# Kernel optimization log

Hardware: AMD Instinct MI355X
Metric: run time of the kernel (lower is better)

## Reference

```python
import jax, jax.numpy as jnp
import numpy as np

B, S, D, FF, E = 4, 2048, 1024, 4096, 8


def setup_inputs() -> dict:
    key = jax.random.key(0)
    ks = jax.random.split(key, 6)
    scale_r = 1.0 / np.sqrt(D)
    return {
        "x": jax.random.normal(ks[0], (B, S, D), dtype=jnp.float32),
        "W_router": jax.random.normal(ks[1], (D, E), dtype=jnp.float32) * scale_r,
        "W1": jax.random.normal(ks[2], (E, D, FF), dtype=jnp.float32) * (1.0 / np.sqrt(D)),
        "b1": jnp.zeros((E, FF), dtype=jnp.float32),
        "W2": jax.random.normal(ks[3], (E, FF, D), dtype=jnp.float32) * (1.0 / np.sqrt(FF)),
        "b2": jnp.zeros((E, D), dtype=jnp.float32),
    }


def reference(x, W_router, W1, b1, W2, b2):
    # Router: softmax over experts, top-2, renormalize the 2 gates with softmax
    logits = jnp.einsum("bsd,de->bse", x, W_router)          # [B,S,E]
    probs = jax.nn.softmax(logits, axis=-1)
    top_vals, top_idx = jax.lax.top_k(probs, 2)               # [B,S,2]
    gates2 = jax.nn.softmax(top_vals, axis=-1)                # [B,S,2]

    num_experts = W1.shape[0]
    out = jnp.zeros_like(x)
    # Faithful masked-dense MoE: each expert runs over all tokens (input masked),
    # output scaled by its gate (0 for non-selected tokens).
    for i in range(num_experts):
        sel = (top_idx == i)                                  # [B,S,2] bool
        mask = jnp.any(sel, axis=-1, keepdims=True).astype(x.dtype)  # [B,S,1]
        xi = x * mask
        h = jax.nn.gelu(jnp.einsum("bsd,df->bsf", xi, W1[i]) + b1[i], approximate=False)
        yi = jnp.einsum("bsf,fd->bsd", h, W2[i]) + b2[i]
        g = jnp.sum(gates2 * sel.astype(x.dtype), axis=-1, keepdims=True)  # [B,S,1]
        out = out + yi * g
    return out
```

## Files before the change

### kernel.cpp

```cpp
#include <hip/hip_runtime.h>
#include <hip/hip_bf16.h>
#include <math.h>

#define NEXP 8
#define DDIM 1024
#define FFDIM 4096
#define NTOK 8192
#define NSLOT (NTOK * 2)
#define BM 128
#define BN 128
#define BK 64
#define MAXT ((NSLOT / BM) + NEXP)

typedef __attribute__((ext_vector_type(8))) __bf16 bf16x8;
typedef __attribute__((ext_vector_type(4))) __bf16 bf16x4;
typedef __attribute__((ext_vector_type(4))) float f32x4;

union BF8 { __bf16 b[8]; uint4 u; bf16x8 v; };

typedef const __attribute__((address_space(1))) void* gptr1_t;
typedef __attribute__((address_space(3))) void* lptr3_t;
__device__ __forceinline__ void gll16(const void* g, void* l) {
    __builtin_amdgcn_global_load_lds((gptr1_t)g, (lptr3_t)l, 16, 0, 0);
}

__device__ __forceinline__ float gelu_fast(float v) {
    float vv = v * v;
    float ex = __expf(v * fmaf(0.0713548162726f, vv, 1.59576912161f));
    float s = __builtin_amdgcn_rcpf(ex + 1.0f);
    return v * (1.0f - s);
}

__device__ __forceinline__ int swz(int row, int colb) {
    return row * 128 + (colb ^ ((row & 7) << 4));
}

__device__ __forceinline__ int xcd_logical(int bid, int nwg) {
    if (nwg & 7) return bid;
    return (bid & 7) * (nwg >> 3) + (bid >> 3);
}

__global__ __launch_bounds__(256)
void router_kernel(const float* __restrict__ x, const float* __restrict__ Wr,
                   __bf16* __restrict__ xb, int write_xb,
                   int* __restrict__ idx2, float* __restrict__ gates2,
                   int* __restrict__ counts)
{
    int tid = threadIdx.x;
    int t = blockIdx.x * 4 + (tid >> 6);
    int lane = tid & 63;
    const float* xr = x + (size_t)t * DDIM;

    float acc[NEXP];
#pragma unroll
    for (int e = 0; e < NEXP; ++e) acc[e] = 0.f;

#pragma unroll
    for (int i = 0; i < 2; ++i) {
        int d0 = i * 512 + lane * 8;
        float4 a = *(const float4*)(xr + d0);
        float4 b = *(const float4*)(xr + d0 + 4);
        float vals[8] = {a.x, a.y, a.z, a.w, b.x, b.y, b.z, b.w};
#pragma unroll
        for (int q = 0; q < 8; ++q) {
            const float* wrow = Wr + (size_t)(d0 + q) * NEXP;
#pragma unroll
            for (int e = 0; e < NEXP; ++e) acc[e] += vals[q] * wrow[e];
        }
        if (write_xb) {
            BF8 pk;
#pragma unroll
            for (int q = 0; q < 8; ++q) pk.b[q] = (__bf16)vals[q];
            *(uint4*)(xb + (size_t)t * DDIM + d0) = pk.u;
        }
    }
#pragma unroll
    for (int e = 0; e < NEXP; ++e) {
        float v = acc[e];
        for (int off = 32; off > 0; off >>= 1) v += __shfl_xor(v, off, 64);
        acc[e] = v;
    }
    if (lane == 0) {
        float mx = acc[0];
#pragma unroll
        for (int e = 1; e < NEXP; ++e) mx = fmaxf(mx, acc[e]);
        float p[NEXP]; float s = 0.f;
#pragma unroll
        for (int e = 0; e < NEXP; ++e) { p[e] = expf(acc[e] - mx); s += p[e]; }
        float inv = 1.f / s;
#pragma unroll
        for (int e = 0; e < NEXP; ++e) p[e] *= inv;
        int i1 = 0; float p1 = p[0];
#pragma unroll
        for (int e = 1; e < NEXP; ++e) if (p[e] > p1) { p1 = p[e]; i1 = e; }
        int i2 = -1; float p2 = -1.f;
#pragma unroll
        for (int e = 0; e < NEXP; ++e) {
            if (e == i1) continue;
            if (p[e] > p2) { p2 = p[e]; i2 = e; }
        }
        float u = expf(p2 - p1);
        float den = 1.f + u;
        idx2[2 * t] = i1; idx2[2 * t + 1] = i2;
        gates2[2 * t] = 1.f / den; gates2[2 * t + 1] = u / den;
        atomicAdd(&counts[i1], 1);
        atomicAdd(&counts[i2], 1);
    }
}

__global__ __launch_bounds__(256)
void offsets_kernel(const int* __restrict__ counts, int* __restrict__ offsets,
                    int* __restrict__ cursors, int* __restrict__ tiletab)
{
    __shared__ int soff[NEXP], stile[NEXP + 1];
    int tid = threadIdx.x;
    if (tid == 0) {
        int off = 0, tt = 0;
        for (int e = 0; e < NEXP; ++e) {
            soff[e] = off; stile[e] = tt;
            int c = counts[e];
            off += c; tt += (c + BM - 1) / BM;
        }
        stile[NEXP] = tt;
    }
    __syncthreads();
    if (tid < NEXP) { offsets[tid] = soff[tid]; cursors[tid] = 0; }
    int total = stile[NEXP];
    for (int i = tid; i < MAXT; i += 256) {
        if (i < total) {
            int e = 0;
            while (stile[e + 1] <= i) ++e;
            tiletab[2 * i] = e; tiletab[2 * i + 1] = i - stile[e];
        } else {
            tiletab[2 * i] = -1; tiletab[2 * i + 1] = 0;
        }
    }
}

__global__ __launch_bounds__(256)
void fill_kernel(const int* __restrict__ idx2, const float* __restrict__ gates2,
                 const int* __restrict__ offsets, int* __restrict__ cursors,
                 int* __restrict__ perm, float* __restrict__ gate_slot,
                 int* __restrict__ tslot)
{
    int t = blockIdx.x * 256 + threadIdx.x;
    if (t >= NTOK) return;
#pragma unroll
    for (int s = 0; s < 2; ++s) {
        int e = idx2[2 * t + s];
        int pos = atomicAdd(&cursors[e], 1);
        int slot = offsets[e] + pos;
        perm[slot] = t;
        gate_slot[slot] = gates2[2 * t + s];
        tslot[2 * t + s] = slot;
    }
}

__global__ __launch_bounds__(128)
void convert_w_kernel(const float* __restrict__ W, __bf16* __restrict__ WT, int K, int N)
{
    int ktiles = K >> 6;
    int nt = blockIdx.x / ktiles;
    int kt = blockIdx.x % ktiles;
    int e = blockIdx.y;
    const float* We = W + (size_t)e * K * N;
    int r = threadIdx.x;
    const float* src = We + (size_t)(kt * 64) * N + nt * 128 + r;
    char* dst = (char*)WT + ((((size_t)e * (N >> 7) + nt) * ktiles + kt) << 14) + r * 128;
    float f[64];
#pragma unroll
    for (int j = 0; j < 64; ++j) f[j] = src[(size_t)j * N];
#pragma unroll
    for (int gi = 0; gi < 8; ++gi) {
        BF8 pk;
#pragma unroll
        for (int q = 0; q < 8; ++q) pk.b[q] = (__bf16)f[gi * 8 + q];
        *(uint4*)(dst + ((gi * 16) ^ ((r & 7) << 4))) = pk.u;
    }
}

__device__ __forceinline__ bool tile_header(const int* counts, const int* offsets,
                                            const int* tiletab, int e_arg, int c_arg, int CH,
                                            int tile_idx,
                                            int& e, int& start, int& cnt, int& hbase, int& row0,
                                            int& rows_here)
{
    int rowtile;
    if (e_arg >= 0) {
        e = e_arg;
        int cbase = c_arg * CH;
        cnt = counts[e] - cbase;
        if (cnt <= 0) return false;
        if (cnt > CH) cnt = CH;
        start = offsets[e] + cbase;
        rowtile = tile_idx;
        hbase = start;
    } else {
        e = tiletab[2 * tile_idx];
        if (e < 0) return false;
        rowtile = tiletab[2 * tile_idx + 1];
        start = offsets[e];
        cnt = counts[e];
        hbase = 0;
    }
    row0 = rowtile * BM;
    if (row0 >= cnt) return false;
    rows_here = cnt - row0;
    if (rows_here > BM) rows_here = BM;
    return true;
}

__global__ __launch_bounds__(256)
void gemm1_fast(const __bf16* __restrict__ xb, const __bf16* __restrict__ W1T,
                const float* __restrict__ b1,
                const int* __restrict__ perm, const int* __restrict__ counts,
                const int* __restrict__ offsets, const int* __restrict__ tiletab,
                __bf16* __restrict__ H, int e_arg, int c_arg, int CH)
{
    __shared__ __align__(16) char smem[(BM + BN) * 128];
    char* As = smem;
    char* Bs = smem + BM * 128;

    int e, start, cnt, hbase, row0, rows_here;
    if (!tile_header(counts, offsets, tiletab, e_arg, c_arg, CH, blockIdx.y,
                     e, start, cnt, hbase, row0, rows_here))
        return;

    const float* b1e = b1 + (size_t)e * FFDIM;
    int nt = blockIdx.x;
    int n0 = nt * BN;
    const char* bsrc = (const char*)W1T + ((((size_t)e * (FFDIM >> 7) + nt) * (DDIM >> 6)) << 14);

    int tid = threadIdx.x;
    int lane = tid & 63;
    int wid = tid >> 6;
    int wm = wid >> 1, wn = wid & 1;
    int lr = lane & 15, lhi = lane >> 4;

    int ar = tid >> 1, ach = tid & 1;
    int token = -1;
    if (ar < rows_here) token = perm[start + row0 + ar];
    const __bf16* arow = xb + (size_t)(token < 0 ? 0 : token) * DDIM + ach * 32;

    const char* bwave = bsrc + wid * 4096 + lane * 16;
    char* bldsb = Bs + wid * 4096;

    f32x4 acc[4][4] = {};

    for (int kt = 0; kt < DDIM / BK; ++kt) {
        __syncthreads();
#pragma unroll
        for (int j = 0; j < 4; ++j)
            gll16(bwave + ((size_t)kt << 14) + j * 1024, bldsb + j * 1024);
        {
            uint4 v[4];
            if (token >= 0) {
                const uint4* p = (const uint4*)(arow + kt * BK);
#pragma unroll
                for (int i = 0; i < 4; ++i) v[i] = p[i];
            } else {
#pragma unroll
                for (int i = 0; i < 4; ++i) v[i] = make_uint4(0u, 0u, 0u, 0u);
            }
#pragma unroll
            for (int i = 0; i < 4; ++i)
                *(uint4*)(As + swz(ar, ach * 64 + i * 16)) = v[i];
        }
        __syncthreads();

#pragma unroll
        for (int kk = 0; kk < 2; ++kk) {
            bf16x8 af[4], bfr[4];
#pragma unroll
            for (int m = 0; m < 4; ++m)
                af[m] = *(const bf16x8*)(As + swz(wm * 64 + m * 16 + lr, kk * 64 + lhi * 16));
#pragma unroll
            for (int n = 0; n < 4; ++n)
                bfr[n] = *(const bf16x8*)(Bs + swz(wn * 64 + n * 16 + lr, kk * 64 + lhi * 16));
#pragma unroll
            for (int m = 0; m < 4; ++m)
#pragma unroll
                for (int n = 0; n < 4; ++n)
                    acc[m][n] = __builtin_amdgcn_mfma_f32_16x16x32_bf16(af[m], bfr[n], acc[m][n], 0, 0, 0);
        }
    }

    float bias[4];
#pragma unroll
    for (int n = 0; n < 4; ++n) bias[n] = b1e[n0 + wn * 64 + n * 16 + lr];

#pragma unroll
    for (int m = 0; m < 4; ++m) {
        int rbase = wm * 64 + m * 16 + lhi * 4;
#pragma unroll
        for (int j = 0; j < 4; ++j) {
            int rl = rbase + j;
            if (rl < rows_here) {
                __bf16* hr = H + (size_t)(start + row0 + rl - hbase) * FFDIM + n0 + wn * 64;
#pragma unroll
                for (int n = 0; n < 4; ++n) {
                    float v = acc[m][n][j] + bias[n];
                    hr[n * 16 + lr] = (__bf16)gelu_fast(v);
                }
            }
        }
    }
}

__global__ __launch_bounds__(256)
void gemm2_fast(const __bf16* __restrict__ H, const __bf16* __restrict__ W2T,
                const float* __restrict__ b2,
                const int* __restrict__ perm, const float* __restrict__ gate_slot,
                const int* __restrict__ counts, const int* __restrict__ offsets,
                const int* __restrict__ tiletab,
                float* __restrict__ out, __bf16* __restrict__ Y, int use_y,
                int e_arg, int c_arg, int CH)
{
    __shared__ __align__(16) char smem[(BM + BN) * 128];
    char* As = smem;
    char* Bs = smem + BM * 128;

    const int NTN = DDIM / BN;
    int tile_idx, nt;
    if (e_arg >= 0) { nt = blockIdx.x; tile_idx = blockIdx.y; }
    else {
        int L = xcd_logical(blockIdx.x, gridDim.x);
        nt = L % NTN;
        tile_idx = L / NTN;
    }

    int e, start, cnt, hbase, row0, rows_here;
    if (!tile_header(counts, offsets, tiletab, e_arg, c_arg, CH, tile_idx,
                     e, start, cnt, hbase, row0, rows_here))
        return;

    const float* b2e = b2 + (size_t)e * DDIM;
    int n0 = nt * BN;
    const char* bsrc = (const char*)W2T + ((((size_t)e * (DDIM >> 7) + nt) * (FFDIM >> 6)) << 14);

    int tid = threadIdx.x;
    int lane = tid & 63;
    int wid = tid >> 6;
    int wm = wid >> 1, wn = wid & 1;
    int lr = lane & 15, lhi = lane >> 4;

    int ar = tid >> 1, ach = tid & 1;
    bool aval = (ar < rows_here);
    const __bf16* hrow = H + (size_t)(aval ? (start + row0 + ar - hbase) : 0) * FFDIM + ach * 32;

    const char* bwave = bsrc + wid * 4096 + lane * 16;
    char* bldsb = Bs + wid * 4096;

    f32x4 acc[4][4] = {};

    for (int kt = 0; kt < FFDIM / BK; ++kt) {
        __syncthreads();
#pragma unroll
        for (int j = 0; j < 4; ++j)
            gll16(bwave + ((size_t)kt << 14) + j * 1024, bldsb + j * 1024);
        {
            uint4 v[4];
            if (aval) {
                const uint4* p = (const uint4*)(hrow + kt * BK);
#pragma unroll
                for (int i = 0; i < 4; ++i) v[i] = p[i];
            } else {
#pragma unroll
                for (int i = 0; i < 4; ++i) v[i] = make_uint4(0u, 0u, 0u, 0u);
            }
#pragma unroll
            for (int i = 0; i < 4; ++i)
                *(uint4*)(As + swz(ar, ach * 64 + i * 16)) = v[i];
        }
        __syncthreads();

#pragma unroll
        for (int kk = 0; kk < 2; ++kk) {
            bf16x8 af[4], bfr[4];
#pragma unroll
            for (int m = 0; m < 4; ++m)
                af[m] = *(const bf16x8*)(As + swz(wm * 64 + m * 16 + lr, kk * 64 + lhi * 16));
#pragma unroll
            for (int n = 0; n < 4; ++n)
                bfr[n] = *(const bf16x8*)(Bs + swz(wn * 64 + n * 16 + lr, kk * 64 + lhi * 16));
#pragma unroll
            for (int m = 0; m < 4; ++m)
#pragma unroll
                for (int n = 0; n < 4; ++n)
                    acc[m][n] = __builtin_amdgcn_mfma_f32_16x16x32_bf16(af[m], bfr[n], acc[m][n], 0, 0, 0);
        }
    }

    float bias[4];
#pragma unroll
    for (int n = 0; n < 4; ++n) bias[n] = b2e[n0 + wn * 64 + n * 16 + lr];

#pragma unroll
    for (int m = 0; m < 4; ++m) {
        int rbase = wm * 64 + m * 16 + lhi * 4;
#pragma unroll
        for (int j = 0; j < 4; ++j) {
            int rl = rbase + j;
            if (rl < rows_here) {
                int slot = start + row0 + rl;
                float g = gate_slot[slot];
                if (use_y) {
                    __bf16* yrow = Y + (size_t)slot * DDIM + n0 + wn * 64;
#pragma unroll
                    for (int n = 0; n < 4; ++n)
                        yrow[n * 16 + lr] = (__bf16)((acc[m][n][j] + bias[n]) * g);
                } else {
                    int token = perm[slot];
                    float* orow = out + (size_t)token * DDIM + n0 + wn * 64;
#pragma unroll
                    for (int n = 0; n < 4; ++n)
                        atomicAdd(orow + n * 16 + lr, (acc[m][n][j] + bias[n]) * g);
                }
            }
        }
    }
}

__global__ __launch_bounds__(256)
void combine_kernel(const __bf16* __restrict__ Y, const int* __restrict__ tslot,
                    float* __restrict__ out)
{
    int t = blockIdx.x;
    int c = threadIdx.x * 4;
    int sa = tslot[2 * t], sb = tslot[2 * t + 1];
    bf16x4 a = *(const bf16x4*)(Y + (size_t)sa * DDIM + c);
    bf16x4 b = *(const bf16x4*)(Y + (size_t)sb * DDIM + c);
    float4 r;
    r.x = (float)a[0] + (float)b[0];
    r.y = (float)a[1] + (float)b[1];
    r.z = (float)a[2] + (float)b[2];
    r.w = (float)a[3] + (float)b[3];
    *(float4*)(out + (size_t)t * DDIM + c) = r;
}

__global__ __launch_bounds__(256)
void gemm1_legacy(const float* __restrict__ x, const float* __restrict__ W1,
                  const float* __restrict__ b1,
                  const int* __restrict__ perm, const int* __restrict__ counts,
                  const int* __restrict__ offsets, const int* __restrict__ tiletab,
                  __bf16* __restrict__ H, int e_arg, int c_arg, int CH)
{
    __shared__ __align__(16) char smem[(BM + BN) * 128];
    char* As = smem;
    char* Bs = smem + BM * 128;

    int e, start, cnt, hbase, row0, rows_here;
    if (!tile_header(counts, offsets, tiletab, e_arg, c_arg, CH, blockIdx.y,
                     e, start, cnt, hbase, row0, rows_here))
        return;

    const float* W1e = W1 + (size_t)e * DDIM * FFDIM;
    const float* b1e = b1 + (size_t)e * FFDIM;
    int n0 = blockIdx.x * BN;

    int tid = threadIdx.x;
    int lane = tid & 63;
    int wid = tid >> 6;
    int wm = wid >> 1, wn = wid & 1;
    int lr = lane & 15, lhi = lane >> 4;

    int ar = tid >> 1, ach = tid & 1;
    int token = -1;
    if (ar < rows_here) token = perm[start + row0 + ar];
    const float* arow = x + (size_t)(token < 0 ? 0 : token) * DDIM + ach * 32;

    int bn = tid & 127, bkh = tid >> 7;
    const float* bcol = W1e + (size_t)bkh * 32 * FFDIM + n0 + bn;

    f32x4 acc[4][4] = {};

    for (int k0 = 0; k0 < DDIM; k0 += BK) {
        __syncthreads();
        {
            BF8 pk[4];
            if (token >= 0) {
                const float4* p = (const float4*)(arow + k0);
#pragma unroll
                for (int i = 0; i < 4; ++i) {
                    float4 v0 = p[2 * i], v1 = p[2 * i + 1];
                    pk[i].b[0] = (__bf16)v0.x; pk[i].b[1] = (__bf16)v0.y;
                    pk[i].b[2] = (__bf16)v0.z; pk[i].b[3] = (__bf16)v0.w;
                    pk[i].b[4] = (__bf16)v1.x; pk[i].b[5] = (__bf16)v1.y;
                    pk[i].b[6] = (__bf16)v1.z; pk[i].b[7] = (__bf16)v1.w;
                }
            } else {
#pragma unroll
                for (int i = 0; i < 4; ++i) pk[i].u = make_uint4(0u, 0u, 0u, 0u);
            }
#pragma unroll
            for (int i = 0; i < 4; ++i)
                *(uint4*)(As + swz(ar, ach * 64 + i * 16)) = pk[i].u;
        }
        {
            float f[32];
            const float* p = bcol + (size_t)k0 * FFDIM;
#pragma unroll
            for (int j = 0; j < 32; ++j) f[j] = p[(size_t)j * FFDIM];
#pragma unroll
            for (int i = 0; i < 4; ++i) {
                BF8 pk;
#pragma unroll
                for (int q = 0; q < 8; ++q) pk.b[q] = (__bf16)f[i * 8 + q];
                *(uint4*)(Bs + swz(bn, bkh * 64 + i * 16)) = pk.u;
            }
        }
        __syncthreads();

#pragma unroll
        for (int kk = 0; kk < 2; ++kk) {
            bf16x8 af[4], bfr[4];
#pragma unroll
            for (int m = 0; m < 4; ++m)
                af[m] = *(const bf16x8*)(As + swz(wm * 64 + m * 16 + lr, kk * 64 + lhi * 16));
#pragma unroll
            for (int n = 0; n < 4; ++n)
                bfr[n] = *(const bf16x8*)(Bs + swz(wn * 64 + n * 16 + lr, kk * 64 + lhi * 16));
#pragma unroll
            for (int m = 0; m < 4; ++m)
#pragma unroll
                for (int n = 0; n < 4; ++n)
                    acc[m][n] = __builtin_amdgcn_mfma_f32_16x16x32_bf16(af[m], bfr[n], acc[m][n], 0, 0, 0);
        }
    }

    float bias[4];
#pragma unroll
    for (int n = 0; n < 4; ++n) bias[n] = b1e[n0 + wn * 64 + n * 16 + lr];

#pragma unroll
    for (int m = 0; m < 4; ++m) {
        int rbase = wm * 64 + m * 16 + lhi * 4;
#pragma unroll
        for (int j = 0; j < 4; ++j) {
            int rl = rbase + j;
            if (rl < rows_here) {
                __bf16* hr = H + (size_t)(start + row0 + rl - hbase) * FFDIM + n0 + wn * 64;
#pragma unroll
                for (int n = 0; n < 4; ++n) {
                    float v = acc[m][n][j] + bias[n];
                    hr[n * 16 + lr] = (__bf16)gelu_fast(v);
                }
            }
        }
    }
}

__global__ __launch_bounds__(256)
void gemm2_legacy(const __bf16* __restrict__ H, const float* __restrict__ W2,
                  const float* __restrict__ b2,
                  const int* __restrict__ perm, const float* __restrict__ gate_slot,
                  const int* __restrict__ counts, const int* __restrict__ offsets,
                  const int* __restrict__ tiletab,
                  float* __restrict__ out, int e_arg, int c_arg, int CH)
{
    __shared__ __align__(16) char smem[(BM + BN) * 128];
    char* As = smem;
    char* Bs = smem + BM * 128;

    int e, start, cnt, hbase, row0, rows_here;
    if (!tile_header(counts, offsets, tiletab, e_arg, c_arg, CH, blockIdx.y,
                     e, start, cnt, hbase, row0, rows_here))
        return;

    const float* W2e = W2 + (size_t)e * FFDIM * DDIM;
    const float* b2e = b2 + (size_t)e * DDIM;
    int n0 = blockIdx.x * BN;

    int tid = threadIdx.x;
    int lane = tid & 63;
    int wid = tid >> 6;
    int wm = wid >> 1, wn = wid & 1;
    int lr = lane & 15, lhi = lane >> 4;

    int ar = tid >> 1, ach = tid & 1;
    bool aval = (ar < rows_here);
    const __bf16* hrow = H + (size_t)(aval ? (start + row0 + ar - hbase) : 0) * FFDIM + ach * 32;

    int bn = tid & 127, bkh = tid >> 7;
    const float* bcol = W2e + (size_t)bkh * 32 * DDIM + n0 + bn;

    f32x4 acc[4][4] = {};

    for (int k0 = 0; k0 < FFDIM; k0 += BK) {
        __syncthreads();
        {
            uint4 v[4];
            if (aval) {
                const uint4* p = (const uint4*)(hrow + k0);
#pragma unroll
                for (int i = 0; i < 4; ++i) v[i] = p[i];
            } else {
#pragma unroll
                for (int i = 0; i < 4; ++i) v[i] = make_uint4(0u, 0u, 0u, 0u);
            }
#pragma unroll
            for (int i = 0; i < 4; ++i)
                *(uint4*)(As + swz(ar, ach * 64 + i * 16)) = v[i];
        }
        {
            float f[32];
            const float* p = bcol + (size_t)k0 * DDIM;
#pragma unroll
            for (int j = 0; j < 32; ++j) f[j] = p[(size_t)j * DDIM];
#pragma unroll
            for (int i = 0; i < 4; ++i) {
                BF8 pk;
#pragma unroll
                for (int q = 0; q < 8; ++q) pk.b[q] = (__bf16)f[i * 8 + q];
                *(uint4*)(Bs + swz(bn, bkh * 64 + i * 16)) = pk.u;
            }
        }
        __syncthreads();

#pragma unroll
        for (int kk = 0; kk < 2; ++kk) {
            bf16x8 af[4], bfr[4];
#pragma unroll
            for (int m = 0; m < 4; ++m)
                af[m] = *(const bf16x8*)(As + swz(wm * 64 + m * 16 + lr, kk * 64 + lhi * 16));
#pragma unroll
            for (int n = 0; n < 4; ++n)
                bfr[n] = *(const bf16x8*)(Bs + swz(wn * 64 + n * 16 + lr, kk * 64 + lhi * 16));
#pragma unroll
            for (int m = 0; m < 4; ++m)
#pragma unroll
                for (int n = 0; n < 4; ++n)
                    acc[m][n] = __builtin_amdgcn_mfma_f32_16x16x32_bf16(af[m], bfr[n], acc[m][n], 0, 0, 0);
        }
    }

    float bias[4];
#pragma unroll
    for (int n = 0; n < 4; ++n) bias[n] = b2e[n0 + wn * 64 + n * 16 + lr];

#pragma unroll
    for (int m = 0; m < 4; ++m) {
        int rbase = wm * 64 + m * 16 + lhi * 4;
#pragma unroll
        for (int j = 0; j < 4; ++j) {
            int rl = rbase + j;
            if (rl < rows_here) {
                int slot = start + row0 + rl;
                int token = perm[slot];
                float g = gate_slot[slot];
                float* orow = out + (size_t)token * DDIM + n0 + wn * 64;
#pragma unroll
                for (int n = 0; n < 4; ++n) {
                    float v = (acc[m][n][j] + bias[n]) * g;
                    atomicAdd(orow + n * 16 + lr, v);
                }
            }
        }
    }
}

extern "C" void kernel_launch(void* const* d_in, const int* in_sizes, int n_in,
                              void* d_out, int out_size, void* d_ws, size_t ws_size,
                              hipStream_t stream)
{
    const float* x  = (const float*)d_in[0];
    const float* Wr = (const float*)d_in[1];
    const float* W1 = (const float*)d_in[2];
    const float* b1 = (const float*)d_in[3];
    const float* W2 = (const float*)d_in[4];
    const float* b2 = (const float*)d_in[5];
    float* out = (float*)d_out;

    char* ws = (char*)d_ws;
    int* counts   = (int*)ws;
    int* offsets  = counts + 8;
    int* cursors  = offsets + 8;
    int* tiletab  = cursors + 8;
    int* idx2     = tiletab + 2 * MAXT;
    float* gates2 = (float*)(idx2 + 2 * NTOK);
    int* perm     = (int*)(gates2 + 2 * NTOK);
    float* gate_slot = (float*)(perm + NSLOT);
    int* tslot    = (int*)(gate_slot + NSLOT);
    char* hraw = (char*)(tslot + 2 * NTOK);
    size_t small_end = (((size_t)(hraw - ws)) + 255) & ~(size_t)255;

    __bf16* xb  = (__bf16*)(ws + small_end);
    __bf16* W1T = xb + (size_t)NTOK * DDIM;
    __bf16* W2T = W1T + (size_t)NEXP * DDIM * FFDIM;
    __bf16* Hf  = W2T + (size_t)NEXP * FFDIM * DDIM;
    __bf16* Y   = W1T;
    size_t fast_off = small_end + ((size_t)NTOK * DDIM + 2 * (size_t)NEXP * DDIM * FFDIM) * 2;
    size_t availHf = ws_size > fast_off ? ws_size - fast_off : 0;
    size_t need_H = (size_t)NSLOT * FFDIM * 2;
    bool have_w = availHf >= (size_t)BM * FFDIM * 2 * 8;

    hipMemsetAsync(counts, 0, 8 * sizeof(int), stream);

    router_kernel<<<NTOK / 4, 256, 0, stream>>>(x, Wr, xb, have_w ? 1 : 0,
                                                idx2, gates2, counts);
    if (have_w) {
        convert_w_kernel<<<dim3((FFDIM / 128) * (DDIM / 64), NEXP), 128, 0, stream>>>(W1, W1T, DDIM, FFDIM);
        convert_w_kernel<<<dim3((DDIM / 128) * (FFDIM / 64), NEXP), 128, 0, stream>>>(W2, W2T, FFDIM, DDIM);
    }
    offsets_kernel<<<1, 256, 0, stream>>>(counts, offsets, cursors, tiletab);
    fill_kernel<<<NTOK / 256, 256, 0, stream>>>(idx2, gates2, offsets, cursors, perm, gate_slot, tslot);

    if (have_w && availHf >= need_H) {
        dim3 g1(FFDIM / BN, MAXT, 1);
        gemm1_fast<<<g1, 256, 0, stream>>>(xb, W1T, b1, perm, counts, offsets, tiletab, Hf, -1, 0, 0);
        gemm2_fast<<<(DDIM / BN) * MAXT, 256, 0, stream>>>(Hf, W2T, b2, perm, gate_slot, counts,
                                                           offsets, tiletab, out, Y, 1, -1, 0, 0);
        combine_kernel<<<NTOK, 256, 0, stream>>>(Y, tslot, out);
    } else if (have_w) {
        hipMemsetAsync(d_out, 0, (size_t)out_size * sizeof(float), stream);
        long long chl = (long long)((availHf / ((size_t)FFDIM * 2)) / BM) * BM;
        int CH = (int)(chl > 4096 ? 4096 : chl);
        int nchunk = (NSLOT + CH - 1) / CH;
        for (int e = 0; e < NEXP; ++e) {
            for (int c = 0; c < nchunk; ++c) {
                dim3 g1(FFDIM / BN, CH / BM, 1);
                gemm1_fast<<<g1, 256, 0, stream>>>(xb, W1T, b1, perm, counts, offsets, tiletab, Hf, e, c, CH);
                dim3 g2(DDIM / BN, CH / BM, 1);
                gemm2_fast<<<g2, 256, 0, stream>>>(Hf, W2T, b2, perm, gate_slot, counts, offsets, tiletab,
                                                   out, (__bf16*)nullptr, 0, e, c, CH);
            }
        }
    } else {
        hipMemsetAsync(d_out, 0, (size_t)out_size * sizeof(float), stream);
        __bf16* H = (__bf16*)(ws + small_end);
        size_t avail = ws_size > small_end ? ws_size - small_end : 0;
        if (avail >= need_H) {
            dim3 g1(FFDIM / BN, MAXT, 1);
            gemm1_legacy<<<g1, 256, 0, stream>>>(x, W1, b1, perm, counts, offsets, tiletab, H, -1, 0, 0);
            dim3 g2(DDIM / BN, MAXT, 1);
            gemm2_legacy<<<g2, 256, 0, stream>>>(H, W2, b2, perm, gate_slot, counts, offsets, tiletab, out, -1, 0, 0);
        } else {
            long long chl = (long long)((avail / ((size_t)FFDIM * 2)) / BM) * BM;
            int CH = (int)(chl > 2048 ? 2048 : chl);
            if (CH >= BM) {
                int nchunk = (NSLOT + CH - 1) / CH;
                for (int e = 0; e < NEXP; ++e) {
                    for (int c = 0; c < nchunk; ++c) {
                        dim3 g1(FFDIM / BN, CH / BM, 1);
                        gemm1_legacy<<<g1, 256, 0, stream>>>(x, W1, b1, perm, counts, offsets, tiletab, H, e, c, CH);
                        dim3 g2(DDIM / BN, CH / BM, 1);
                        gemm2_legacy<<<g2, 256, 0, stream>>>(H, W2, b2, perm, gate_slot, counts, offsets, tiletab, out, e, c, CH);
                    }
                }
            }
        }
    }
}
```

Measured before the change: 791.6 us.

## Load A operand fragments directly from global memory, bypassing LDS staging

Both grouped GEMM kernels now skip staging the gathered A tile (tokens or hidden rows) in shared memory. Each wave reads its MFMA A fragments straight from global memory through per-row pointers, and shared memory holds only the B tile. This removes the LDS store/load round-trip for A and halves shared memory use. In exchange, A rows are re-read from global/L2 by the two wn waves and the loads sit on the MFMA critical path without prefetch, so latency may be exposed.

```diff
diff --git a/kernel.cpp b/kernel.cpp
--- a/kernel.cpp
+++ b/kernel.cpp
@@ -217,9 +217,7 @@
                 const int* __restrict__ offsets, const int* __restrict__ tiletab,
                 __bf16* __restrict__ H, int e_arg, int c_arg, int CH)
 {
-    __shared__ __align__(16) char smem[(BM + BN) * 128];
-    char* As = smem;
-    char* Bs = smem + BM * 128;
+    __shared__ __align__(16) char Bs[BN * 128];
 
     int e, start, cnt, hbase, row0, rows_here;
     if (!tile_header(counts, offsets, tiletab, e_arg, c_arg, CH, blockIdx.y,
@@ -237,10 +235,13 @@
     int wm = wid >> 1, wn = wid & 1;
     int lr = lane & 15, lhi = lane >> 4;
 
-    int ar = tid >> 1, ach = tid & 1;
-    int token = -1;
-    if (ar < rows_here) token = perm[start + row0 + ar];
-    const __bf16* arow = xb + (size_t)(token < 0 ? 0 : token) * DDIM + ach * 32;
+    const char* aptr[4];
+#pragma unroll
+    for (int m = 0; m < 4; ++m) {
+        int grow = wm * 64 + m * 16 + lr;
+        int idx = start + row0 + (grow < rows_here ? grow : 0);
+        aptr[m] = (const char*)(xb + (size_t)perm[idx] * DDIM);
+    }
 
     const char* bwave = bsrc + wid * 4096 + lane * 16;
     char* bldsb = Bs + wid * 4096;
@@ -252,20 +253,6 @@
 #pragma unroll
         for (int j = 0; j < 4; ++j)
             gll16(bwave + ((size_t)kt << 14) + j * 1024, bldsb + j * 1024);
-        {
-            uint4 v[4];
-            if (token >= 0) {
-                const uint4* p = (const uint4*)(arow + kt * BK);
-#pragma unroll
-                for (int i = 0; i < 4; ++i) v[i] = p[i];
-            } else {
-#pragma unroll
-                for (int i = 0; i < 4; ++i) v[i] = make_uint4(0u, 0u, 0u, 0u);
-            }
-#pragma unroll
-            for (int i = 0; i < 4; ++i)
-                *(uint4*)(As + swz(ar, ach * 64 + i * 16)) = v[i];
-        }
         __syncthreads();
 
 #pragma unroll
@@ -273,7 +260,7 @@
             bf16x8 af[4], bfr[4];
 #pragma unroll
             for (int m = 0; m < 4; ++m)
-                af[m] = *(const bf16x8*)(As + swz(wm * 64 + m * 16 + lr, kk * 64 + lhi * 16));
+                af[m] = *(const bf16x8*)(aptr[m] + kt * 128 + kk * 64 + lhi * 16);
 #pragma unroll
             for (int n = 0; n < 4; ++n)
                 bfr[n] = *(const bf16x8*)(Bs + swz(wn * 64 + n * 16 + lr, kk * 64 + lhi * 16));
@@ -316,9 +303,7 @@
                 float* __restrict__ out, __bf16* __restrict__ Y, int use_y,
                 int e_arg, int c_arg, int CH)
 {
-    __shared__ __align__(16) char smem[(BM + BN) * 128];
-    char* As = smem;
-    char* Bs = smem + BM * 128;
+    __shared__ __align__(16) char Bs[BN * 128];
 
     const int NTN = DDIM / BN;
     int tile_idx, nt;
@@ -344,9 +329,13 @@
     int wm = wid >> 1, wn = wid & 1;
     int lr = lane & 15, lhi = lane >> 4;
 
-    int ar = tid >> 1, ach = tid & 1;
-    bool aval = (ar < rows_here);
-    const __bf16* hrow = H + (size_t)(aval ? (start + row0 + ar - hbase) : 0) * FFDIM + ach * 32;
+    const char* aptr[4];
+#pragma unroll
+    for (int m = 0; m < 4; ++m) {
+        int grow = wm * 64 + m * 16 + lr;
+        int r = (grow < rows_here ? grow : 0);
+        aptr[m] = (const char*)(H + (size_t)(start + row0 + r - hbase) * FFDIM);
+    }
 
     const char* bwave = bsrc + wid * 4096 + lane * 16;
     char* bldsb = Bs + wid * 4096;
@@ -358,20 +347,6 @@
 #pragma unroll
         for (int j = 0; j < 4; ++j)
             gll16(bwave + ((size_t)kt << 14) + j * 1024, bldsb + j * 1024);
-        {
-            uint4 v[4];
-            if (aval) {
-                const uint4* p = (const uint4*)(hrow + kt * BK);
-#pragma unroll
-                for (int i = 0; i < 4; ++i) v[i] = p[i];
-            } else {
-#pragma unroll
-                for (int i = 0; i < 4; ++i) v[i] = make_uint4(0u, 0u, 0u, 0u);
-            }
-#pragma unroll
-            for (int i = 0; i < 4; ++i)
-                *(uint4*)(As + swz(ar, ach * 64 + i * 16)) = v[i];
-        }
         __syncthreads();
 
 #pragma unroll
@@ -379,7 +354,7 @@
             bf16x8 af[4], bfr[4];
 #pragma unroll
             for (int m = 0; m < 4; ++m)
-                af[m] = *(const bf16x8*)(As + swz(wm * 64 + m * 16 + lr, kk * 64 + lhi * 16));
+                af[m] = *(const bf16x8*)(aptr[m] + kt * 128 + kk * 64 + lhi * 16);
 #pragma unroll
             for (int n = 0; n < 4; ++n)
                 bfr[n] = *(const bf16x8*)(Bs + swz(wn * 64 + n * 16 + lr, kk * 64 + lhi * 16));
```

Result: slower. 1.167 ms (+47.4%).

## Double-buffer LDS tiles in gemm2 to overlap global loads with MFMA

Applied to the files above, without the earlier changes.

The second expert GEMM kernel now uses two LDS buffers for the A and B tiles. It prefetches the next K tile (async global_load_lds for W2 and register loads for H) while running MFMA on the current one, and drops one __syncthreads per iteration. The goal is to hide global memory latency behind compute. In exchange, LDS use doubles, which can lower occupancy, and the prefetched A values stay in registers across the MFMA loop.

```diff
diff --git a/kernel.cpp b/kernel.cpp
--- a/kernel.cpp
+++ b/kernel.cpp
@@ -316,9 +316,8 @@
                 float* __restrict__ out, __bf16* __restrict__ Y, int use_y,
                 int e_arg, int c_arg, int CH)
 {
-    __shared__ __align__(16) char smem[(BM + BN) * 128];
-    char* As = smem;
-    char* Bs = smem + BM * 128;
+    __shared__ __align__(16) char AsB[2][BM * 128];
+    __shared__ __align__(16) char BsB[2][BN * 128];
 
     const int NTN = DDIM / BN;
     int tile_idx, nt;
@@ -349,46 +348,76 @@
     const __bf16* hrow = H + (size_t)(aval ? (start + row0 + ar - hbase) : 0) * FFDIM + ach * 32;
 
     const char* bwave = bsrc + wid * 4096 + lane * 16;
-    char* bldsb = Bs + wid * 4096;
-
+    int swzA[4];
+#pragma unroll
+    for (int i = 0; i < 4; ++i) swzA[i] = swz(ar, ach * 64 + i * 16);
+
+    const int NT = FFDIM / BK;
     f32x4 acc[4][4] = {};
 
-    for (int kt = 0; kt < FFDIM / BK; ++kt) {
+    {
+#pragma unroll
+        for (int j = 0; j < 4; ++j)
+            gll16(bwave, BsB[0] + wid * 4096 + j * 1024), bwave += 1024;
+        bwave -= 4096;
+        uint4 v[4];
+        if (aval) {
+            const uint4* p = (const uint4*)hrow;
+#pragma unroll
+            for (int i = 0; i < 4; ++i) v[i] = p[i];
+        } else {
+#pragma unroll
+            for (int i = 0; i < 4; ++i) v[i] = make_uint4(0u, 0u, 0u, 0u);
+        }
+#pragma unroll
+        for (int i = 0; i < 4; ++i)
+            *(uint4*)(AsB[0] + swzA[i]) = v[i];
+    }
+
+    int cur = 0;
+    for (int kt = 0; kt < NT; ++kt) {
         __syncthreads();
-#pragma unroll
-        for (int j = 0; j < 4; ++j)
-            gll16(bwave + ((size_t)kt << 14) + j * 1024, bldsb + j * 1024);
-        {
-            uint4 v[4];
+        bool pf = (kt + 1 < NT);
+        uint4 v[4];
+        if (pf) {
+            const char* tsrc = bwave + ((size_t)(kt + 1) << 14);
+#pragma unroll
+            for (int j = 0; j < 4; ++j)
+                gll16(tsrc + j * 1024, BsB[cur ^ 1] + wid * 4096 + j * 1024);
             if (aval) {
-                const uint4* p = (const uint4*)(hrow + kt * BK);
+                const uint4* p = (const uint4*)(hrow + (kt + 1) * BK);
 #pragma unroll
                 for (int i = 0; i < 4; ++i) v[i] = p[i];
             } else {
 #pragma unroll
                 for (int i = 0; i < 4; ++i) v[i] = make_uint4(0u, 0u, 0u, 0u);
             }
-#pragma unroll
-            for (int i = 0; i < 4; ++i)
-                *(uint4*)(As + swz(ar, ach * 64 + i * 16)) = v[i];
-        }
-        __syncthreads();
-
+        }
+
+        const char* Ac = AsB[cur];
+        const char* Bc = BsB[cur];
 #pragma unroll
         for (int kk = 0; kk < 2; ++kk) {
             bf16x8 af[4], bfr[4];
 #pragma unroll
             for (int m = 0; m < 4; ++m)
-                af[m] = *(const bf16x8*)(As + swz(wm * 64 + m * 16 + lr, kk * 64 + lhi * 16));
+                af[m] = *(const bf16x8*)(Ac + swz(wm * 64 + m * 16 + lr, kk * 64 + lhi * 16));
 #pragma unroll
             for (int n = 0; n < 4; ++n)
-                bfr[n] = *(const bf16x8*)(Bs + swz(wn * 64 + n * 16 + lr, kk * 64 + lhi * 16));
+                bfr[n] = *(const bf16x8*)(Bc + swz(wn * 64 + n * 16 + lr, kk * 64 + lhi * 16));
 #pragma unroll
             for (int m = 0; m < 4; ++m)
 #pragma unroll
                 for (int n = 0; n < 4; ++n)
                     acc[m][n] = __builtin_amdgcn_mfma_f32_16x16x32_bf16(af[m], bfr[n], acc[m][n], 0, 0, 0);
         }
+
+        if (pf) {
+#pragma unroll
+            for (int i = 0; i < 4; ++i)
+                *(uint4*)(AsB[cur ^ 1] + swzA[i]) = v[i];
+        }
+        cur ^= 1;
     }
 
     float bias[4];
```

Result: slower. 861.6 us (+8.8%).
